# Kernel tuning notes

Hardware: AMD Instinct MI355X
Metric: run time of the kernel (lower is better)

The kernel has to match this reference:

```python
import jax, jax.numpy as jnp
import numpy as np

NUM_HEADS = 4
LN_EPS = 1e-5


def setup_inputs() -> dict:
    key = jax.random.key(0)
    ks = jax.random.split(key, 5)
    C = 256
    x = jax.random.normal(ks[0], (2, C, 64, 64), dtype=jnp.float32)
    in_proj_w = jax.random.normal(ks[1], (3 * C, C), dtype=jnp.float32) * (1.0 / np.sqrt(C))
    in_proj_b = jax.random.normal(ks[2], (3 * C,), dtype=jnp.float32) * 0.02
    out_w = jax.random.normal(ks[3], (C, C), dtype=jnp.float32) * (1.0 / np.sqrt(C))
    out_b = jax.random.normal(ks[4], (C,), dtype=jnp.float32) * 0.02
    ln_g = jnp.ones((C,), dtype=jnp.float32)
    ln_b = jnp.zeros((C,), dtype=jnp.float32)
    return {"x": x, "in_proj_w": in_proj_w, "in_proj_b": in_proj_b,
            "out_w": out_w, "out_b": out_b, "ln_g": ln_g, "ln_b": ln_b}


def reference(x, in_proj_w, in_proj_b, out_w, out_b, ln_g, ln_b):
    b, c, H, W = x.shape
    S = H * W  # 4096 == max_tokens -> no pooling, no interpolation
    hd = c // NUM_HEADS
    t = x.reshape(b, c, S).transpose(0, 2, 1)  # (b, S, c)
    # fused QKV projection (in_proj_weight is [3c, c], rows = q,k,v blocks)
    qkv = t @ in_proj_w.T + in_proj_b  # (b, S, 3c)
    q, k, v = jnp.split(qkv, 3, axis=-1)
    def to_heads(a):
        return a.reshape(b, S, NUM_HEADS, hd).transpose(0, 2, 1, 3)  # (b, h, S, d)
    q = to_heads(q) * (1.0 / np.sqrt(hd))
    k = to_heads(k)
    v = to_heads(v)
    scores = jnp.einsum('bhqd,bhkd->bhqk', q, k)      # (b, h, S, S)
    probs = jax.nn.softmax(scores, axis=-1)
    attn = jnp.einsum('bhqk,bhkd->bhqd', probs, v)    # (b, h, S, d)
    attn = attn.transpose(0, 2, 1, 3).reshape(b, S, c)
    out = attn @ out_w.T + out_b                      # output projection
    # LayerNorm over channel dim
    mu = jnp.mean(out, axis=-1, keepdims=True)
    var = jnp.mean(jnp.square(out - mu), axis=-1, keepdims=True)
    out = (out - mu) * jax.lax.rsqrt(var + LN_EPS) * ln_g + ln_b
    return out.transpose(0, 2, 1).reshape(b, c, H, W)
```

## Files before the change

### kernel.cpp

```cpp
#include <hip/hip_runtime.h>
#include <cstddef>

#define S_TOK 4096
#define CDIM 256
#define NHEADS 4
#define HDIM 64
#define LSK 72
#define LDA 36
#define LDY 264
#define LOG2E 1.44269504f

typedef __attribute__((ext_vector_type(8))) short short8;
typedef __attribute__((ext_vector_type(4))) float floatx4;

__device__ inline unsigned short f2bf(float f) {
  union { float f; unsigned u; } v;
  v.f = f;
  unsigned r = v.u + 0x7fff + ((v.u >> 16) & 1);
  return (unsigned short)(r >> 16);
}
__device__ inline float bf2f(unsigned short u) {
  union { unsigned u; float f; } v;
  v.u = ((unsigned)u) << 16;
  return v.f;
}
__device__ inline unsigned pack_bf16(float a, float b) {
#if __has_builtin(__builtin_amdgcn_cvt_pk_bf16_f32)
  typedef __bf16 bf16x2 __attribute__((ext_vector_type(2)));
  union { bf16x2 v; unsigned u; } r;
  r.v = __builtin_amdgcn_cvt_pk_bf16_f32(a, b);
  return r.u;
#else
  unsigned r;
  asm("v_cvt_pk_bf16_f32 %0, %1, %2" : "=v"(r) : "v"(a), "v"(b));
  return r;
#endif
}

__device__ inline void pl32swap(unsigned& a, unsigned& b) {
  asm("v_permlane32_swap_b32 %0, %1" : "+v"(a), "+v"(b));
}
__device__ inline void pl16swap(unsigned& a, unsigned& b) {
  asm("v_permlane16_swap_b32 %0, %1" : "+v"(a), "+v"(b));
}

__global__ __launch_bounds__(256) void convert_w_kernel(
    const float* __restrict__ ipw, const float* __restrict__ ow,
    unsigned short* __restrict__ wbf) {
  int e = (blockIdx.x * 256 + threadIdx.x) * 8;
  const float* src = (e < 196608) ? (ipw + e) : (ow + (e - 196608));
  float4 f0 = *(const float4*)(src);
  float4 f1 = *(const float4*)(src + 4);
  uint4 u;
  u.x = pack_bf16(f0.x, f0.y);
  u.y = pack_bf16(f0.z, f0.w);
  u.z = pack_bf16(f1.x, f1.y);
  u.w = pack_bf16(f1.z, f1.w);
  *(uint4*)(wbf + e) = u;
}

__global__ __launch_bounds__(256) void qkv_gemm_kernel(
    const float* __restrict__ x, const unsigned short* __restrict__ wip,
    const float* __restrict__ ipb, unsigned short* __restrict__ q16,
    unsigned short* __restrict__ k16, unsigned short* __restrict__ vt16) {
  __shared__ __align__(16) unsigned short As[64 * LDA];
  __shared__ __align__(16) unsigned short Bs[3][64 * LDA];
  const int tid = threadIdx.x;
  const int wave = tid >> 6, lane = tid & 63;
  const int quad = lane >> 4, l16 = lane & 15;
  const int n0 = blockIdx.x * 64;
  const int tok0 = blockIdx.y * 64;
  const int b = blockIdx.z;

  const int c_l = tid >> 3, t8 = tid & 7;
  const float* gx = x + (((size_t)(b * CDIM + c_l)) << 12) + tok0 + t8 * 8;
  unsigned short* wa = &As[(t8 * 8) * LDA + c_l];

  const int rr = tid >> 2, c4 = tid & 3;
  const unsigned short* gw0 = wip + (size_t)(n0 + rr) * CDIM + c4 * 8;
  unsigned short* wb0 = &Bs[0][rr * LDA + c4 * 8];

  floatx4 acc[3][4];
#pragma unroll
  for (int s = 0; s < 3; ++s)
#pragma unroll
    for (int nt = 0; nt < 4; ++nt) acc[s][nt] = (floatx4){0.f, 0.f, 0.f, 0.f};

  float4 a0 = *(const float4*)(gx);
  float4 a1 = *(const float4*)(gx + 4);
  uint4 bp[3];
#pragma unroll
  for (int s = 0; s < 3; ++s)
    bp[s] = *(const uint4*)(gw0 + (size_t)s * 256 * CDIM);

  for (int ks = 0; ks < 8; ++ks) {
    __syncthreads();
    {
      unsigned p;
      p = pack_bf16(a0.x, a0.y);
      wa[0 * LDA] = (unsigned short)p; wa[1 * LDA] = (unsigned short)(p >> 16);
      p = pack_bf16(a0.z, a0.w);
      wa[2 * LDA] = (unsigned short)p; wa[3 * LDA] = (unsigned short)(p >> 16);
      p = pack_bf16(a1.x, a1.y);
      wa[4 * LDA] = (unsigned short)p; wa[5 * LDA] = (unsigned short)(p >> 16);
      p = pack_bf16(a1.z, a1.w);
      wa[6 * LDA] = (unsigned short)p; wa[7 * LDA] = (unsigned short)(p >> 16);
    }
#pragma unroll
    for (int s = 0; s < 3; ++s) {
      unsigned short* w = wb0 + s * 64 * LDA;
      *(uint2*)w = (uint2){bp[s].x, bp[s].y};
      *(uint2*)(w + 4) = (uint2){bp[s].z, bp[s].w};
    }
    __syncthreads();
    if (ks < 7) {
      const float* gxn = gx + ((size_t)((ks + 1) * 32) << 12);
      a0 = *(const float4*)(gxn);
      a1 = *(const float4*)(gxn + 4);
#pragma unroll
      for (int s = 0; s < 3; ++s)
        bp[s] = *(const uint4*)(gw0 + (size_t)s * 256 * CDIM + (ks + 1) * 32);
    }
    short8 af = *(const short8*)&As[(wave * 16 + l16) * LDA + quad * 8];
#pragma unroll
    for (int s = 0; s < 3; ++s)
#pragma unroll
      for (int nt = 0; nt < 4; ++nt) {
        short8 bf = *(const short8*)&Bs[s][(nt * 16 + l16) * LDA + quad * 8];
        acc[s][nt] = __builtin_amdgcn_mfma_f32_16x16x32_bf16(af, bf, acc[s][nt], 0, 0, 0);
      }
  }

  const float qsc = 0.125f * LOG2E;
#pragma unroll
  for (int nt = 0; nt < 4; ++nt) {
    int cb = n0 + nt * 16 + l16;
    int h = cb >> 6, dh = cb & 63;
    float bq = ipb[cb], bk = ipb[256 + cb], bv = ipb[512 + cb];
    size_t base = ((size_t)(b * NHEADS + h)) * S_TOK;
#pragma unroll
    for (int r = 0; r < 4; ++r) {
      int tok = tok0 + wave * 16 + quad * 4 + r;
      q16[(base + tok) * HDIM + dh] = f2bf((acc[0][nt][r] + bq) * qsc);
      k16[(base + tok) * HDIM + dh] = f2bf(acc[1][nt][r] + bk);
    }
    int tokv = tok0 + wave * 16 + quad * 4;
    uint2 u;
    u.x = pack_bf16(acc[2][nt][0] + bv, acc[2][nt][1] + bv);
    u.y = pack_bf16(acc[2][nt][2] + bv, acc[2][nt][3] + bv);
    *(uint2*)&vt16[((size_t)(b * NHEADS + h) * HDIM + dh) * S_TOK + tokv] = u;
  }
}

__global__ __launch_bounds__(256) void attn_kernel(
    const unsigned short* __restrict__ q16,
    const unsigned short* __restrict__ k16,
    const unsigned short* __restrict__ vt16,
    unsigned short* __restrict__ op, float* __restrict__ lp) {
  __shared__ __align__(16) unsigned short Ks[2][64 * LSK];
  __shared__ __align__(16) unsigned short Vt[2][64 * LSK];

  const int tid = threadIdx.x;
  const int wave = tid >> 6;
  const int lane = tid & 63;
  const int quad = lane >> 4;
  const int l16 = lane & 15;
  const int bh = blockIdx.y;
  const int q0 = blockIdx.x * 256;
  const int split = blockIdx.z;
  const int kt0 = split * 16;

  short8 qf[4][2];
#pragma unroll
  for (int mt = 0; mt < 4; ++mt) {
    const unsigned short* qg =
        q16 + ((size_t)bh * S_TOK + q0 + wave * 64 + mt * 16 + l16) * HDIM + quad * 8;
    qf[mt][0] = *(const short8*)(qg);
    qf[mt][1] = *(const short8*)(qg + 32);
  }

  const int sr = tid >> 3, scc = tid & 7;
  const unsigned short* kg = k16 + ((size_t)bh * S_TOK + sr) * HDIM + scc * 8;
  const unsigned short* vg = vt16 + ((size_t)bh * HDIM + sr) * S_TOK + scc * 8;

  floatx4 O[4][4];
  float lsum[4] = {0.f, 0.f, 0.f, 0.f};
#pragma unroll
  for (int mt = 0; mt < 4; ++mt)
#pragma unroll
    for (int nt = 0; nt < 4; ++nt) O[mt][nt] = (floatx4){0.f, 0.f, 0.f, 0.f};

  uint4 k0r = *(const uint4*)(kg + (size_t)kt0 * 64 * HDIM);
  uint4 k1r = *(const uint4*)(kg + (size_t)kt0 * 64 * HDIM + 32 * HDIM);
  uint4 v0r = *(const uint4*)(vg + kt0 * 64);
  uint4 v1r = *(const uint4*)(vg + kt0 * 64 + (size_t)32 * S_TOK);
  {
    unsigned short* kw = &Ks[0][sr * LSK + scc * 8];
    unsigned short* vw = &Vt[0][sr * LSK + scc * 8];
    *(uint4*)kw = k0r;
    *(uint4*)(kw + 32 * LSK) = k1r;
    *(uint4*)vw = v0r;
    *(uint4*)(vw + 32 * LSK) = v1r;
  }
  __syncthreads();

  for (int t = 0; t < 16; ++t) {
    const int cur = t & 1;
    if (t < 15) {
      const unsigned short* kgn = kg + (size_t)(kt0 + t + 1) * 64 * HDIM;
      const unsigned short* vgn = vg + (kt0 + t + 1) * 64;
      k0r = *(const uint4*)(kgn);
      k1r = *(const uint4*)(kgn + 32 * HDIM);
      v0r = *(const uint4*)(vgn);
      v1r = *(const uint4*)(vgn + (size_t)32 * S_TOK);
    }
    const unsigned short* Kb = Ks[cur];
    const unsigned short* Vb = Vt[cur];

#pragma unroll
    for (int c = 0; c < 2; ++c) {
      short8 kfA0 = *(const short8*)(&Kb[((c * 2) * 16 + l16) * LSK + quad * 8]);
      short8 kfA1 = *(const short8*)(&Kb[((c * 2) * 16 + l16) * LSK + 32 + quad * 8]);
      short8 kfB0 = *(const short8*)(&Kb[((c * 2 + 1) * 16 + l16) * LSK + quad * 8]);
      short8 kfB1 = *(const short8*)(&Kb[((c * 2 + 1) * 16 + l16) * LSK + 32 + quad * 8]);
      short8 vf[4];
#pragma unroll
      for (int nt = 0; nt < 4; ++nt)
        vf[nt] = *(const short8*)(&Vb[(nt * 16 + l16) * LSK + c * 32 + quad * 8]);
#pragma unroll
      for (int mt = 0; mt < 4; ++mt) {
        __builtin_amdgcn_s_setprio(1);
        floatx4 cA = (floatx4){0.f, 0.f, 0.f, 0.f};
        cA = __builtin_amdgcn_mfma_f32_16x16x32_bf16(kfA0, qf[mt][0], cA, 0, 0, 0);
        cA = __builtin_amdgcn_mfma_f32_16x16x32_bf16(kfA1, qf[mt][1], cA, 0, 0, 0);
        floatx4 cB = (floatx4){0.f, 0.f, 0.f, 0.f};
        cB = __builtin_amdgcn_mfma_f32_16x16x32_bf16(kfB0, qf[mt][0], cB, 0, 0, 0);
        cB = __builtin_amdgcn_mfma_f32_16x16x32_bf16(kfB1, qf[mt][1], cB, 0, 0, 0);
        __builtin_amdgcn_s_setprio(0);
        float a0 = __builtin_amdgcn_exp2f(cA[0]);
        float a1 = __builtin_amdgcn_exp2f(cA[1]);
        float a2 = __builtin_amdgcn_exp2f(cA[2]);
        float a3 = __builtin_amdgcn_exp2f(cA[3]);
        float b0 = __builtin_amdgcn_exp2f(cB[0]);
        float b1 = __builtin_amdgcn_exp2f(cB[1]);
        float b2 = __builtin_amdgcn_exp2f(cB[2]);
        float b3 = __builtin_amdgcn_exp2f(cB[3]);
        lsum[mt] += ((a0 + a1) + (a2 + a3)) + ((b0 + b1) + (b2 + b3));
        unsigned A0 = pack_bf16(a0, a1), B0 = pack_bf16(a2, a3);
        unsigned A1 = pack_bf16(b0, b1), B1 = pack_bf16(b2, b3);
        pl32swap(A0, A1); pl16swap(A0, A1);
        pl32swap(B0, B1); pl16swap(B0, B1);
        union { uint4 u; short8 s; } pf;
        pf.u.x = A0; pf.u.y = B0; pf.u.z = A1; pf.u.w = B1;
        __builtin_amdgcn_s_setprio(1);
#pragma unroll
        for (int nt = 0; nt < 4; ++nt)
          O[mt][nt] = __builtin_amdgcn_mfma_f32_16x16x32_bf16(pf.s, vf[nt], O[mt][nt], 0, 0, 0);
        __builtin_amdgcn_s_setprio(0);
      }
    }

    if (t < 15) {
      unsigned short* kw = &Ks[cur ^ 1][sr * LSK + scc * 8];
      unsigned short* vw = &Vt[cur ^ 1][sr * LSK + scc * 8];
      *(uint4*)kw = k0r;
      *(uint4*)(kw + 32 * LSK) = k1r;
      *(uint4*)vw = v0r;
      *(uint4*)(vw + 32 * LSK) = v1r;
      __syncthreads();
    }
  }

  const int b = bh >> 2, h = bh & 3;
  unsigned short* op_s = op + (size_t)split * 2097152;
  float* lp_s = lp + (size_t)split * 32768;
#pragma unroll
  for (int mt = 0; mt < 4; ++mt) {
    float ls = lsum[mt];
    ls += __shfl_xor(ls, 16);
    ls += __shfl_xor(ls, 32);
    if (quad == 0)
      lp_s[bh * S_TOK + q0 + wave * 64 + mt * 16 + l16] = ls;
#pragma unroll
    for (int r = 0; r < 4; ++r) {
      int row = q0 + wave * 64 + mt * 16 + quad * 4 + r;
#pragma unroll
      for (int nt = 0; nt < 4; ++nt)
        op_s[((size_t)(b * S_TOK + row)) * CDIM + h * HDIM + nt * 16 + l16] =
            f2bf(O[mt][nt][r]);
    }
  }
}

__device__ inline uint2 merge4(const unsigned short* op, size_t off, float rinv) {
  float s0 = 0.f, s1 = 0.f, s2 = 0.f, s3 = 0.f;
#pragma unroll
  for (int sp = 0; sp < 4; ++sp) {
    uint2 u = *(const uint2*)(op + (size_t)sp * 2097152 + off);
    s0 += bf2f((unsigned short)(u.x & 0xffff));
    s1 += bf2f((unsigned short)(u.x >> 16));
    s2 += bf2f((unsigned short)(u.y & 0xffff));
    s3 += bf2f((unsigned short)(u.y >> 16));
  }
  uint2 r;
  r.x = pack_bf16(s0 * rinv, s1 * rinv);
  r.y = pack_bf16(s2 * rinv, s3 * rinv);
  return r;
}

__global__ __launch_bounds__(256) void out_ln_gemm_kernel(
    const unsigned short* __restrict__ op, const float* __restrict__ lp,
    const unsigned short* __restrict__ wow, const float* __restrict__ obias,
    const float* __restrict__ lng, const float* __restrict__ lnb,
    float* __restrict__ out) {
  __shared__ __align__(16) unsigned short As[16 * LDA];
  __shared__ __align__(16) unsigned short Bs[256 * LDA];
  __shared__ __align__(16) float ys[16 * LDY];
  __shared__ float rsum[64];
  const int tid = threadIdx.x;
  const int wave = tid >> 6, lane = tid & 63;
  const int quad = lane >> 4, l16 = lane & 15;
  const int tok0 = blockIdx.x * 16;

  if (tid < 64) {
    int t = tid >> 2, h = tid & 3;
    int bb = tok0 >> 12;
    int idx = (bb * 4 + h) * 4096 + (tok0 & 4095) + t;
    rsum[tid] =
        1.0f / (lp[idx] + lp[32768 + idx] + lp[65536 + idx] + lp[98304 + idx]);
  }
  __syncthreads();

  const int ar = tid >> 3, ac = tid & 7;
  const size_t abase = (size_t)(tok0 + ar) * CDIM + ac * 4;
  unsigned short* wAp = &As[ar * LDA + ac * 4];
  const int rr = tid >> 2, c4 = tid & 3;
  const unsigned short* gB = wow + (size_t)rr * CDIM + c4 * 8;
  unsigned short* wBp = &Bs[rr * LDA + c4 * 8];

  floatx4 acc[4];
#pragma unroll
  for (int nt = 0; nt < 4; ++nt) acc[nt] = (floatx4){0.f, 0.f, 0.f, 0.f};

  uint2 ap;
  if (tid < 128) ap = merge4(op, abase, rsum[(ar << 2)]);
  uint4 bp[4];
#pragma unroll
  for (int i = 0; i < 4; ++i)
    bp[i] = *(const uint4*)(gB + (size_t)i * 64 * CDIM);

  for (int ks = 0; ks < 8; ++ks) {
    __syncthreads();
    if (tid < 128) *(uint2*)wAp = ap;
#pragma unroll
    for (int i = 0; i < 4; ++i) {
      unsigned short* w = wBp + i * 64 * LDA;
      *(uint2*)w = (uint2){bp[i].x, bp[i].y};
      *(uint2*)(w + 4) = (uint2){bp[i].z, bp[i].w};
    }
    __syncthreads();
    if (ks < 7) {
      int off = (ks + 1) * 32;
      if (tid < 128) {
        int ch = off + ac * 4;
        ap = merge4(op, abase + off, rsum[(ar << 2) + (ch >> 6)]);
      }
#pragma unroll
      for (int i = 0; i < 4; ++i)
        bp[i] = *(const uint4*)(gB + (size_t)i * 64 * CDIM + off);
    }
    short8 af = *(const short8*)&As[l16 * LDA + quad * 8];
    short8 bf[4];
#pragma unroll
    for (int nt = 0; nt < 4; ++nt)
      bf[nt] = *(const short8*)&Bs[(wave * 64 + nt * 16 + l16) * LDA + quad * 8];
#pragma unroll
    for (int nt = 0; nt < 4; ++nt)
      acc[nt] = __builtin_amdgcn_mfma_f32_16x16x32_bf16(af, bf[nt], acc[nt], 0, 0, 0);
  }

#pragma unroll
  for (int nt = 0; nt < 4; ++nt) {
    int c = wave * 64 + nt * 16 + l16;
    float bo = obias[c];
#pragma unroll
    for (int r = 0; r < 4; ++r)
      ys[(quad * 4 + r) * LDY + c] = acc[nt][r] + bo;
  }
  __syncthreads();

  const int gtok = tid >> 4, lf = tid & 15;
  float sum = 0.f, ssq = 0.f;
#pragma unroll
  for (int i = 0; i < 16; ++i) {
    float v = ys[gtok * LDY + i * 16 + lf];
    sum += v;
    ssq += v * v;
  }
  sum += __shfl_xor(sum, 1); ssq += __shfl_xor(ssq, 1);
  sum += __shfl_xor(sum, 2); ssq += __shfl_xor(ssq, 2);
  sum += __shfl_xor(sum, 4); ssq += __shfl_xor(ssq, 4);
  sum += __shfl_xor(sum, 8); ssq += __shfl_xor(ssq, 8);
  float mu = sum * (1.f / 256.f);
  float var = ssq * (1.f / 256.f) - mu * mu;
  float rstd = rsqrtf(var + 1e-5f);
  const int b2 = tok0 >> 12;
  const int sl = (tok0 & 4095) + gtok;
#pragma unroll
  for (int i = 0; i < 16; ++i) {
    int c = i * 16 + lf;
    float v = ys[gtok * LDY + c];
    out[(((size_t)(b2 * CDIM + c)) << 12) + sl] = (v - mu) * rstd * lng[c] + lnb[c];
  }
}

extern "C" void kernel_launch(void* const* d_in, const int* in_sizes, int n_in,
                              void* d_out, int out_size, void* d_ws, size_t ws_size,
                              hipStream_t stream) {
  const float* x = (const float*)d_in[0];
  const float* ipw = (const float*)d_in[1];
  const float* ipb = (const float*)d_in[2];
  const float* ow = (const float*)d_in[3];
  const float* ob = (const float*)d_in[4];
  const float* lng = (const float*)d_in[5];
  const float* lnb = (const float*)d_in[6];
  float* out = (float*)d_out;
  unsigned short* q16 = (unsigned short*)d_ws;
  unsigned short* k16 = q16 + 2097152;
  unsigned short* vt16 = k16 + 2097152;
  unsigned short* op = vt16 + 2097152;
  float* lp = (float*)(op + 8388608);
  unsigned short* wbf = (unsigned short*)(lp + 131072);
  unsigned short* wip = wbf;
  unsigned short* wow = wbf + 196608;

  convert_w_kernel<<<128, 256, 0, stream>>>(ipw, ow, wbf);
  qkv_gemm_kernel<<<dim3(4, 64, 2), 256, 0, stream>>>(x, wip, ipb, q16, k16, vt16);
  attn_kernel<<<dim3(16, 8, 4), 256, 0, stream>>>(q16, k16, vt16, op, lp);
  out_ln_gemm_kernel<<<512, 256, 0, stream>>>(op, lp, wow, ob, lng, lnb, out);
}
```

Before: 153.1 us.

## Remove setprio hints in attention and double token tile in out-proj LN kernel

The attention inner loop no longer raises wave priority around its MFMA groups. The output-projection+LayerNorm kernel now handles 32 tokens per block instead of 16, so all 256 threads load A tiles and each weight tile is reused across two MFMA row tiles, with half as many blocks launched. The LayerNorm reduction is reshaped to 8 lanes per token. The bigger tile cuts redundant weight loads but lowers block-level parallelism and raises register and LDS use.

```diff
diff --git a/kernel.cpp b/kernel.cpp
--- a/kernel.cpp
+++ b/kernel.cpp
@@ -229,14 +229,12 @@
         vf[nt] = *(const short8*)(&Vb[(nt * 16 + l16) * LSK + c * 32 + quad * 8]);
 #pragma unroll
       for (int mt = 0; mt < 4; ++mt) {
-        __builtin_amdgcn_s_setprio(1);
         floatx4 cA = (floatx4){0.f, 0.f, 0.f, 0.f};
         cA = __builtin_amdgcn_mfma_f32_16x16x32_bf16(kfA0, qf[mt][0], cA, 0, 0, 0);
         cA = __builtin_amdgcn_mfma_f32_16x16x32_bf16(kfA1, qf[mt][1], cA, 0, 0, 0);
         floatx4 cB = (floatx4){0.f, 0.f, 0.f, 0.f};
         cB = __builtin_amdgcn_mfma_f32_16x16x32_bf16(kfB0, qf[mt][0], cB, 0, 0, 0);
         cB = __builtin_amdgcn_mfma_f32_16x16x32_bf16(kfB1, qf[mt][1], cB, 0, 0, 0);
-        __builtin_amdgcn_s_setprio(0);
         float a0 = __builtin_amdgcn_exp2f(cA[0]);
         float a1 = __builtin_amdgcn_exp2f(cA[1]);
         float a2 = __builtin_amdgcn_exp2f(cA[2]);
@@ -252,11 +250,9 @@
         pl32swap(B0, B1); pl16swap(B0, B1);
         union { uint4 u; short8 s; } pf;
         pf.u.x = A0; pf.u.y = B0; pf.u.z = A1; pf.u.w = B1;
-        __builtin_amdgcn_s_setprio(1);
 #pragma unroll
         for (int nt = 0; nt < 4; ++nt)
           O[mt][nt] = __builtin_amdgcn_mfma_f32_16x16x32_bf16(pf.s, vf[nt], O[mt][nt], 0, 0, 0);
-        __builtin_amdgcn_s_setprio(0);
       }
     }
 
@@ -313,16 +309,16 @@
     const unsigned short* __restrict__ wow, const float* __restrict__ obias,
     const float* __restrict__ lng, const float* __restrict__ lnb,
     float* __restrict__ out) {
-  __shared__ __align__(16) unsigned short As[16 * LDA];
+  __shared__ __align__(16) unsigned short As[32 * LDA];
   __shared__ __align__(16) unsigned short Bs[256 * LDA];
-  __shared__ __align__(16) float ys[16 * LDY];
-  __shared__ float rsum[64];
+  __shared__ __align__(16) float ys[32 * LDY];
+  __shared__ float rsum[128];
   const int tid = threadIdx.x;
   const int wave = tid >> 6, lane = tid & 63;
   const int quad = lane >> 4, l16 = lane & 15;
-  const int tok0 = blockIdx.x * 16;
-
-  if (tid < 64) {
+  const int tok0 = blockIdx.x * 32;
+
+  if (tid < 128) {
     int t = tid >> 2, h = tid & 3;
     int bb = tok0 >> 12;
     int idx = (bb * 4 + h) * 4096 + (tok0 & 4095) + t;
@@ -338,12 +334,13 @@
   const unsigned short* gB = wow + (size_t)rr * CDIM + c4 * 8;
   unsigned short* wBp = &Bs[rr * LDA + c4 * 8];
 
-  floatx4 acc[4];
-#pragma unroll
-  for (int nt = 0; nt < 4; ++nt) acc[nt] = (floatx4){0.f, 0.f, 0.f, 0.f};
-
-  uint2 ap;
-  if (tid < 128) ap = merge4(op, abase, rsum[(ar << 2)]);
+  floatx4 acc[2][4];
+#pragma unroll
+  for (int mt = 0; mt < 2; ++mt)
+#pragma unroll
+    for (int nt = 0; nt < 4; ++nt) acc[mt][nt] = (floatx4){0.f, 0.f, 0.f, 0.f};
+
+  uint2 ap = merge4(op, abase, rsum[(ar << 2) + (ac >> 4)]);
   uint4 bp[4];
 #pragma unroll
   for (int i = 0; i < 4; ++i)
@@ -351,7 +348,7 @@
 
   for (int ks = 0; ks < 8; ++ks) {
     __syncthreads();
-    if (tid < 128) *(uint2*)wAp = ap;
+    *(uint2*)wAp = ap;
 #pragma unroll
     for (int i = 0; i < 4; ++i) {
       unsigned short* w = wBp + i * 64 * LDA;
@@ -361,54 +358,57 @@
     __syncthreads();
     if (ks < 7) {
       int off = (ks + 1) * 32;
-      if (tid < 128) {
-        int ch = off + ac * 4;
-        ap = merge4(op, abase + off, rsum[(ar << 2) + (ch >> 6)]);
-      }
+      int ch = off + ac * 4;
+      ap = merge4(op, abase + off, rsum[(ar << 2) + (ch >> 6)]);
 #pragma unroll
       for (int i = 0; i < 4; ++i)
         bp[i] = *(const uint4*)(gB + (size_t)i * 64 * CDIM + off);
     }
-    short8 af = *(const short8*)&As[l16 * LDA + quad * 8];
-    short8 bf[4];
+    short8 af[2], bf[4];
+#pragma unroll
+    for (int mt = 0; mt < 2; ++mt)
+      af[mt] = *(const short8*)&As[(mt * 16 + l16) * LDA + quad * 8];
 #pragma unroll
     for (int nt = 0; nt < 4; ++nt)
       bf[nt] = *(const short8*)&Bs[(wave * 64 + nt * 16 + l16) * LDA + quad * 8];
 #pragma unroll
-    for (int nt = 0; nt < 4; ++nt)
-      acc[nt] = __builtin_amdgcn_mfma_f32_16x16x32_bf16(af, bf[nt], acc[nt], 0, 0, 0);
-  }
-
-#pragma unroll
-  for (int nt = 0; nt < 4; ++nt) {
-    int c = wave * 64 + nt * 16 + l16;
-    float bo = obias[c];
-#pragma unroll
-    for (int r = 0; r < 4; ++r)
-      ys[(quad * 4 + r) * LDY + c] = acc[nt][r] + bo;
-  }
+    for (int mt = 0; mt < 2; ++mt)
+#pragma unroll
+      for (int nt = 0; nt < 4; ++nt)
+        acc[mt][nt] = __builtin_amdgcn_mfma_f32_16x16x32_bf16(af[mt], bf[nt], acc[mt][nt], 0, 0, 0);
+  }
+
+#pragma unroll
+  for (int mt = 0; mt < 2; ++mt)
+#pragma unroll
+    for (int nt = 0; nt < 4; ++nt) {
+      int c = wave * 64 + nt * 16 + l16;
+      float bo = obias[c];
+#pragma unroll
+      for (int r = 0; r < 4; ++r)
+        ys[(mt * 16 + quad * 4 + r) * LDY + c] = acc[mt][nt][r] + bo;
+    }
   __syncthreads();
 
-  const int gtok = tid >> 4, lf = tid & 15;
+  const int gtok = tid >> 3, l8 = tid & 7;
   float sum = 0.f, ssq = 0.f;
 #pragma unroll
-  for (int i = 0; i < 16; ++i) {
-    float v = ys[gtok * LDY + i * 16 + lf];
+  for (int i = 0; i < 32; ++i) {
+    float v = ys[gtok * LDY + i * 8 + l8];
     sum += v;
     ssq += v * v;
   }
   sum += __shfl_xor(sum, 1); ssq += __shfl_xor(ssq, 1);
   sum += __shfl_xor(sum, 2); ssq += __shfl_xor(ssq, 2);
   sum += __shfl_xor(sum, 4); ssq += __shfl_xor(ssq, 4);
-  sum += __shfl_xor(sum, 8); ssq += __shfl_xor(ssq, 8);
   float mu = sum * (1.f / 256.f);
   float var = ssq * (1.f / 256.f) - mu * mu;
   float rstd = rsqrtf(var + 1e-5f);
   const int b2 = tok0 >> 12;
   const int sl = (tok0 & 4095) + gtok;
 #pragma unroll
-  for (int i = 0; i < 16; ++i) {
-    int c = i * 16 + lf;
+  for (int i = 0; i < 32; ++i) {
+    int c = i * 8 + l8;
     float v = ys[gtok * LDY + c];
     out[(((size_t)(b2 * CDIM + c)) << 12) + sl] = (v - mu) * rstd * lng[c] + lnb[c];
   }
@@ -437,5 +437,5 @@
   convert_w_kernel<<<128, 256, 0, stream>>>(ipw, ow, wbf);
   qkv_gemm_kernel<<<dim3(4, 64, 2), 256, 0, stream>>>(x, wip, ipb, q16, k16, vt16);
   attn_kernel<<<dim3(16, 8, 4), 256, 0, stream>>>(q16, k16, vt16, op, lp);
-  out_ln_gemm_kernel<<<512, 256, 0, stream>>>(op, lp, wow, ob, lng, lnb, out);
-}
+  out_ln_gemm_kernel<<<256, 256, 0, stream>>>(op, lp, wow, ob, lng, lnb, out);
+}
```

Result: faster. 146.1 us (-4.6%).
